# Performance work log

Hardware: AMD Instinct MI355X
Metric: run time of the kernel (lower is better)

The kernel has to match this reference:

```python
import jax, jax.numpy as jnp
import numpy as np

B, T, C = 4, 2048, 1024
QH = 4            # n_q_heads
D = C // QH       # per-head dim = 256
EPS = 1e-5


def setup_inputs() -> dict:
    key = jax.random.key(0)
    k1, k2, k3 = jax.random.split(key, 3)
    residual = jax.random.normal(k1, (B, T, C), dtype=jnp.float32)
    # scale weights ~ Xavier-ish so relu(score)^2 stays numerically sane
    w_fc = jax.random.normal(k2, (C, C), dtype=jnp.float32) * (1.0 / np.sqrt(C))
    w_proj = jax.random.normal(k3, (C, C), dtype=jnp.float32) * (1.0 / np.sqrt(C))
    ln_g = jnp.ones((C,), dtype=jnp.float32)
    ln_b = jnp.zeros((C,), dtype=jnp.float32)
    return {"residual": residual, "w_fc": w_fc, "w_proj": w_proj,
            "ln_g": ln_g, "ln_b": ln_b}


def _layernorm(x, g, b):
    mu = jnp.mean(x, axis=-1, keepdims=True)
    var = jnp.mean(jnp.square(x - mu), axis=-1, keepdims=True)
    return (x - mu) * jax.lax.rsqrt(var + EPS) * g + b


def reference(residual, w_fc, w_proj, ln_g, ln_b):
    Bx, Tx, Cx = residual.shape
    x = _layernorm(residual, ln_g, ln_b)
    # q: (B, QH, T, D)
    q = x.reshape(Bx, Tx, QH, D).transpose(0, 2, 1, 3)
    # keys: rows of w_fc chopped into 4C kv entries of dim D, shared across heads
    k = w_fc.reshape(-1, D)          # (S, D), S = 4C
    # values: columns of w_proj (i.e. w_proj^T rows) chopped the same way
    v = w_proj.T.reshape(-1, D)      # (S, D)
    scores = jnp.einsum('bhtd,sd->bhts', q, k)
    # softmax(log(relusq(score))) then *exp(lse) == plain relu(score)^2 weights
    p = jnp.square(jax.nn.relu(scores))
    out = jnp.einsum('bhts,sd->bhtd', p, v)
    out = out.transpose(0, 2, 1, 3).reshape(Bx, Tx, Cx)
    return residual + out
```

## Files before the change

kernel.cpp:

```cpp
#include <hip/hip_runtime.h>
#include <hip/hip_bf16.h>

typedef __attribute__((ext_vector_type(8))) short bf16x8;
typedef __attribute__((ext_vector_type(4))) float f32x4;

#define C_    1024
#define MROWS 32768
#define D_    256
#define S_TOT 4096
#define SCH   32
#define NCH   (S_TOT / SCH)

__device__ __forceinline__ unsigned short f2bf(float f) {
  union { float f; unsigned int u; } v; v.f = f;
  unsigned int u = v.u;
  u += 0x7fffu + ((u >> 16) & 1u);
  return (unsigned short)(u >> 16);
}

__device__ __forceinline__ void async16(const void* g, void* l) {
  __builtin_amdgcn_global_load_lds(
      (const __attribute__((address_space(1))) unsigned int*)g,
      (__attribute__((address_space(3))) unsigned int*)l, 16, 0, 0);
}

__global__ __launch_bounds__(256) void ln_kernel(const float* __restrict__ res,
                                                 const float* __restrict__ g,
                                                 const float* __restrict__ b,
                                                 unsigned short* __restrict__ xq) {
  int wave = threadIdx.x >> 6, lane = threadIdx.x & 63;
  int row = blockIdx.x * 4 + wave;
  const float* r = res + (size_t)row * C_;
  float4 x[4];
  float s = 0.f, s2 = 0.f;
  #pragma unroll
  for (int i = 0; i < 4; ++i) {
    x[i] = *(const float4*)(r + i * 256 + lane * 4);
    s  += x[i].x + x[i].y + x[i].z + x[i].w;
    s2 += x[i].x * x[i].x + x[i].y * x[i].y + x[i].z * x[i].z + x[i].w * x[i].w;
  }
  #pragma unroll
  for (int off = 32; off > 0; off >>= 1) {
    s  += __shfl_xor(s, off, 64);
    s2 += __shfl_xor(s2, off, 64);
  }
  float mu  = s * (1.0f / C_);
  float var = s2 * (1.0f / C_) - mu * mu;
  float rs  = rsqrtf(var + 1e-5f);
  #pragma unroll
  for (int i = 0; i < 4; ++i) {
    int c = i * 256 + lane * 4;
    float4 gg = *(const float4*)(g + c);
    float4 bb = *(const float4*)(b + c);
    unsigned short o[4];
    o[0] = f2bf((x[i].x - mu) * rs * gg.x + bb.x);
    o[1] = f2bf((x[i].y - mu) * rs * gg.y + bb.y);
    o[2] = f2bf((x[i].z - mu) * rs * gg.z + bb.z);
    o[3] = f2bf((x[i].w - mu) * rs * gg.w + bb.w);
    *(ushort4*)(xq + (size_t)row * C_ + c) = *(ushort4*)o;
  }
}

__global__ __launch_bounds__(256) void prep_k(const float* __restrict__ wfc,
                                              unsigned short* __restrict__ kq) {
  int t = blockIdx.x * 256 + threadIdx.x;
  int lane = t & 63;
  int sn  = (t >> 6) & 1;
  int kc  = (t >> 7) & 7;
  int sc2 = t >> 10;
  int s = sc2 * 32 + sn * 16 + (lane & 15);
  int d = kc * 32 + (lane >> 4) * 8;
  const float* src = wfc + (size_t)s * D_ + d;
  float4 a = *(const float4*)src;
  float4 b = *(const float4*)(src + 4);
  unsigned short o[8] = { f2bf(a.x), f2bf(a.y), f2bf(a.z), f2bf(a.w),
                          f2bf(b.x), f2bf(b.y), f2bf(b.z), f2bf(b.w) };
  *(uint4*)(kq + (size_t)t * 8) = *(uint4*)o;
}

__global__ __launch_bounds__(256) void prep_v(const float* __restrict__ wproj,
                                              unsigned short* __restrict__ vq) {
  __shared__ unsigned short tile[8192];
  int b = blockIdx.x;
  int tid = threadIdx.x;
  int c0 = b * 8;
  #pragma unroll
  for (int it = 0; it < 4; ++it) {
    int row = it * 256 + tid;
    const float* src = wproj + (size_t)row * C_ + c0;
    float4 a = *(const float4*)src;
    float4 bb = *(const float4*)(src + 4);
    unsigned short* dst = &tile[row * 8];
    dst[0] = f2bf(a.x);  dst[1] = f2bf(a.y);  dst[2] = f2bf(a.z);  dst[3] = f2bf(a.w);
    dst[4] = f2bf(bb.x); dst[5] = f2bf(bb.y); dst[6] = f2bf(bb.z); dst[7] = f2bf(bb.w);
  }
  __syncthreads();
  #pragma unroll
  for (int it = 0; it < 4; ++it) {
    int slot = it * 256 + tid;
    int lane = slot & 63;
    int dn   = slot >> 6;
    int d = dn * 16 + (lane & 15);
    int sl0 = (lane >> 4) * 8;
    unsigned short o[8];
    #pragma unroll
    for (int j = 0; j < 8; ++j) {
      int sl = sl0 + j;
      o[j] = tile[((sl & 3) * 256 + d) * 8 + (sl >> 2)];
    }
    *(uint4*)(vq + (size_t)b * 8192 + (size_t)slot * 8) = *(uint4*)o;
  }
}

__global__ __launch_bounds__(512, 2) void mlpmha_main(
    const unsigned short* __restrict__ xq,
    const unsigned short* __restrict__ kq,
    const unsigned short* __restrict__ vq,
    const float* __restrict__ res,
    float* __restrict__ out) {
  __shared__ unsigned short ldsK[2][8192];
  __shared__ unsigned short ldsV[8192];
  __shared__ unsigned short ldsP[128][36];

  int tid  = threadIdx.x;
  int wave = tid >> 6;
  int lane = tid & 63;
  int l16  = lane & 15;
  int quad = lane >> 4;
  int wgM  = blockIdx.x * 128;

  int mi = wave & 3, si = wave >> 2;
  int ni = wave & 3, mi2 = wave >> 2;

  bf16x8 qf[2][8];
  #pragma unroll
  for (int mt = 0; mt < 2; ++mt) {
    const unsigned short* qr =
        xq + (size_t)(wgM + mi * 32 + mt * 16 + l16) * D_ + quad * 8;
    #pragma unroll
    for (int kc = 0; kc < 8; ++kc) qf[mt][kc] = *(const bf16x8*)(qr + kc * 32);
  }

  f32x4 acc[4][4];
  #pragma unroll
  for (int i = 0; i < 4; ++i)
    #pragma unroll
    for (int j = 0; j < 4; ++j) acc[i][j] = (f32x4){0.f, 0.f, 0.f, 0.f};

  int soff = tid * 8;

  {
    const unsigned short* kg = kq + soff;
    async16(kg, &ldsK[0][soff]);
    async16(kg + 4096, &ldsK[0][soff + 4096]);
  }
  __syncthreads();

  for (int sc = 0; sc < NCH; ++sc) {
    int cur = sc & 1;

    {
      const unsigned short* vg = vq + (size_t)sc * 8192 + soff;
      async16(vg, &ldsV[soff]);
      async16(vg + 4096, &ldsV[soff + 4096]);
    }

    f32x4 sacc[2];
    sacc[0] = (f32x4){0.f, 0.f, 0.f, 0.f};
    sacc[1] = (f32x4){0.f, 0.f, 0.f, 0.f};
    #pragma unroll
    for (int kc = 0; kc < 8; ++kc) {
      bf16x8 kb = *(const bf16x8*)&ldsK[cur][(kc * 2 + si) * 512 + lane * 8];
      #pragma unroll
      for (int mt = 0; mt < 2; ++mt)
        sacc[mt] = __builtin_amdgcn_mfma_f32_16x16x32_bf16(qf[mt][kc], kb, sacc[mt], 0, 0, 0);
    }

    #pragma unroll
    for (int mt = 0; mt < 2; ++mt)
      #pragma unroll
      for (int r = 0; r < 4; ++r) {
        float v = sacc[mt][r];
        v = v > 0.f ? v * v : 0.f;
        ldsP[mi * 32 + mt * 16 + quad * 4 + r][si * 16 + l16] = f2bf(v);
      }

    __syncthreads();

    if (sc + 1 < NCH) {
      const unsigned short* kg = kq + (size_t)(sc + 1) * 8192 + soff;
      async16(kg, &ldsK[1 - cur][soff]);
      async16(kg + 4096, &ldsK[1 - cur][soff + 4096]);
    }

    {
      bf16x8 vb[4];
      #pragma unroll
      for (int dnl = 0; dnl < 4; ++dnl)
        vb[dnl] = *(const bf16x8*)&ldsV[((ni * 4 + dnl) * 64 + lane) * 8];
      #pragma unroll
      for (int mt2 = 0; mt2 < 4; ++mt2) {
        const unsigned short* pp = &ldsP[mi2 * 64 + mt2 * 16 + l16][quad * 8];
        union { ushort4 h[2]; bf16x8 v; } pu;
        pu.h[0] = *(const ushort4*)pp;
        pu.h[1] = *(const ushort4*)(pp + 4);
        bf16x8 pa = pu.v;
        #pragma unroll
        for (int dnl = 0; dnl < 4; ++dnl)
          acc[mt2][dnl] = __builtin_amdgcn_mfma_f32_16x16x32_bf16(pa, vb[dnl], acc[mt2][dnl], 0, 0, 0);
      }
    }

    __syncthreads();
  }

  #pragma unroll
  for (int mt2 = 0; mt2 < 4; ++mt2)
    #pragma unroll
    for (int r = 0; r < 4; ++r) {
      size_t row = (size_t)(wgM + mi2 * 64 + mt2 * 16 + quad * 4 + r) * D_;
      #pragma unroll
      for (int dnl = 0; dnl < 4; ++dnl) {
        size_t idx = row + ni * 64 + dnl * 16 + l16;
        out[idx] = res[idx] + acc[mt2][dnl][r];
      }
    }
}

extern "C" void kernel_launch(void* const* d_in, const int* in_sizes, int n_in,
                              void* d_out, int out_size, void* d_ws, size_t ws_size,
                              hipStream_t stream) {
  const float* res   = (const float*)d_in[0];
  const float* wfc   = (const float*)d_in[1];
  const float* wproj = (const float*)d_in[2];
  const float* g     = (const float*)d_in[3];
  const float* b     = (const float*)d_in[4];
  float* out = (float*)d_out;

  unsigned short* xq = (unsigned short*)d_ws;
  unsigned short* kq = xq + (size_t)MROWS * D_;
  unsigned short* vq = kq + (size_t)S_TOT * D_;

  ln_kernel<<<2048, 256, 0, stream>>>(res, g, b, xq);
  prep_k<<<512, 256, 0, stream>>>(wfc, kq);
  prep_v<<<128, 256, 0, stream>>>(wproj, vq);
  mlpmha_main<<<256, 512, 0, stream>>>(xq, kq, vq, res, out);
}
```

Baseline: 242.7 us.

## Double S-chunk to 64 and fuse prep kernels into one launch

The main attention-like kernel now processes 64 kv entries per iteration instead of 32. Each wave covers 64 query rows and a 16-wide S slice, which doubles register-held Q fragments and K/V/P LDS buffers, and halves the number of barrier-separated iterations. The three preprocessing kernels (layernorm, K reformat, V transpose) are merged into one launch that dispatches on block index, removing two launch gaps. The larger LDS footprint and register pressure (qf grows to 32 vectors) may reduce occupancy below the requested two blocks per CU.

Result: slower. 256.7 us (+5.8%).

```diff
diff --git a/kernel.cpp b/kernel.cpp
--- a/kernel.cpp
+++ b/kernel.cpp
@@ -8,7 +8,7 @@
 #define MROWS 32768
 #define D_    256
 #define S_TOT 4096
-#define SCH   32
+#define SCH   64
 #define NCH   (S_TOT / SCH)
 
 __device__ __forceinline__ unsigned short f2bf(float f) {
@@ -24,91 +24,91 @@
       (__attribute__((address_space(3))) unsigned int*)l, 16, 0, 0);
 }
 
-__global__ __launch_bounds__(256) void ln_kernel(const float* __restrict__ res,
-                                                 const float* __restrict__ g,
-                                                 const float* __restrict__ b,
-                                                 unsigned short* __restrict__ xq) {
-  int wave = threadIdx.x >> 6, lane = threadIdx.x & 63;
-  int row = blockIdx.x * 4 + wave;
-  const float* r = res + (size_t)row * C_;
-  float4 x[4];
-  float s = 0.f, s2 = 0.f;
-  #pragma unroll
-  for (int i = 0; i < 4; ++i) {
-    x[i] = *(const float4*)(r + i * 256 + lane * 4);
-    s  += x[i].x + x[i].y + x[i].z + x[i].w;
-    s2 += x[i].x * x[i].x + x[i].y * x[i].y + x[i].z * x[i].z + x[i].w * x[i].w;
-  }
-  #pragma unroll
-  for (int off = 32; off > 0; off >>= 1) {
-    s  += __shfl_xor(s, off, 64);
-    s2 += __shfl_xor(s2, off, 64);
-  }
-  float mu  = s * (1.0f / C_);
-  float var = s2 * (1.0f / C_) - mu * mu;
-  float rs  = rsqrtf(var + 1e-5f);
-  #pragma unroll
-  for (int i = 0; i < 4; ++i) {
-    int c = i * 256 + lane * 4;
-    float4 gg = *(const float4*)(g + c);
-    float4 bb = *(const float4*)(b + c);
-    unsigned short o[4];
-    o[0] = f2bf((x[i].x - mu) * rs * gg.x + bb.x);
-    o[1] = f2bf((x[i].y - mu) * rs * gg.y + bb.y);
-    o[2] = f2bf((x[i].z - mu) * rs * gg.z + bb.z);
-    o[3] = f2bf((x[i].w - mu) * rs * gg.w + bb.w);
-    *(ushort4*)(xq + (size_t)row * C_ + c) = *(ushort4*)o;
-  }
-}
-
-__global__ __launch_bounds__(256) void prep_k(const float* __restrict__ wfc,
-                                              unsigned short* __restrict__ kq) {
-  int t = blockIdx.x * 256 + threadIdx.x;
-  int lane = t & 63;
-  int sn  = (t >> 6) & 1;
-  int kc  = (t >> 7) & 7;
-  int sc2 = t >> 10;
-  int s = sc2 * 32 + sn * 16 + (lane & 15);
-  int d = kc * 32 + (lane >> 4) * 8;
-  const float* src = wfc + (size_t)s * D_ + d;
-  float4 a = *(const float4*)src;
-  float4 b = *(const float4*)(src + 4);
-  unsigned short o[8] = { f2bf(a.x), f2bf(a.y), f2bf(a.z), f2bf(a.w),
-                          f2bf(b.x), f2bf(b.y), f2bf(b.z), f2bf(b.w) };
-  *(uint4*)(kq + (size_t)t * 8) = *(uint4*)o;
-}
-
-__global__ __launch_bounds__(256) void prep_v(const float* __restrict__ wproj,
-                                              unsigned short* __restrict__ vq) {
+__global__ __launch_bounds__(256) void prep_all(
+    const float* __restrict__ res, const float* __restrict__ g,
+    const float* __restrict__ b, const float* __restrict__ wfc,
+    const float* __restrict__ wproj,
+    unsigned short* __restrict__ xq, unsigned short* __restrict__ kq,
+    unsigned short* __restrict__ vq) {
   __shared__ unsigned short tile[8192];
-  int b = blockIdx.x;
+  int bid = blockIdx.x;
   int tid = threadIdx.x;
-  int c0 = b * 8;
-  #pragma unroll
-  for (int it = 0; it < 4; ++it) {
-    int row = it * 256 + tid;
-    const float* src = wproj + (size_t)row * C_ + c0;
+
+  if (bid < 2048) {
+    int wave = tid >> 6, lane = tid & 63;
+    int row = bid * 4 + wave;
+    const float* r = res + (size_t)row * C_;
+    float4 x[4];
+    float s = 0.f, s2 = 0.f;
+    #pragma unroll
+    for (int i = 0; i < 4; ++i) {
+      x[i] = *(const float4*)(r + i * 256 + lane * 4);
+      s  += x[i].x + x[i].y + x[i].z + x[i].w;
+      s2 += x[i].x * x[i].x + x[i].y * x[i].y + x[i].z * x[i].z + x[i].w * x[i].w;
+    }
+    #pragma unroll
+    for (int off = 32; off > 0; off >>= 1) {
+      s  += __shfl_xor(s, off, 64);
+      s2 += __shfl_xor(s2, off, 64);
+    }
+    float mu  = s * (1.0f / C_);
+    float var = s2 * (1.0f / C_) - mu * mu;
+    float rs  = rsqrtf(var + 1e-5f);
+    #pragma unroll
+    for (int i = 0; i < 4; ++i) {
+      int c = i * 256 + lane * 4;
+      float4 gg = *(const float4*)(g + c);
+      float4 bb = *(const float4*)(b + c);
+      unsigned short o[4];
+      o[0] = f2bf((x[i].x - mu) * rs * gg.x + bb.x);
+      o[1] = f2bf((x[i].y - mu) * rs * gg.y + bb.y);
+      o[2] = f2bf((x[i].z - mu) * rs * gg.z + bb.z);
+      o[3] = f2bf((x[i].w - mu) * rs * gg.w + bb.w);
+      *(ushort4*)(xq + (size_t)row * C_ + c) = *(ushort4*)o;
+    }
+  } else if (bid < 2560) {
+    int t = (bid - 2048) * 256 + tid;
+    int lane = t & 63;
+    int sn  = (t >> 6) & 1;
+    int kc  = (t >> 7) & 7;
+    int sc2 = t >> 10;
+    int s = sc2 * 32 + sn * 16 + (lane & 15);
+    int d = kc * 32 + (lane >> 4) * 8;
+    const float* src = wfc + (size_t)s * D_ + d;
     float4 a = *(const float4*)src;
-    float4 bb = *(const float4*)(src + 4);
-    unsigned short* dst = &tile[row * 8];
-    dst[0] = f2bf(a.x);  dst[1] = f2bf(a.y);  dst[2] = f2bf(a.z);  dst[3] = f2bf(a.w);
-    dst[4] = f2bf(bb.x); dst[5] = f2bf(bb.y); dst[6] = f2bf(bb.z); dst[7] = f2bf(bb.w);
-  }
-  __syncthreads();
-  #pragma unroll
-  for (int it = 0; it < 4; ++it) {
-    int slot = it * 256 + tid;
-    int lane = slot & 63;
-    int dn   = slot >> 6;
-    int d = dn * 16 + (lane & 15);
-    int sl0 = (lane >> 4) * 8;
-    unsigned short o[8];
-    #pragma unroll
-    for (int j = 0; j < 8; ++j) {
-      int sl = sl0 + j;
-      o[j] = tile[((sl & 3) * 256 + d) * 8 + (sl >> 2)];
-    }
-    *(uint4*)(vq + (size_t)b * 8192 + (size_t)slot * 8) = *(uint4*)o;
+    float4 b2 = *(const float4*)(src + 4);
+    unsigned short o[8] = { f2bf(a.x), f2bf(a.y), f2bf(a.z), f2bf(a.w),
+                            f2bf(b2.x), f2bf(b2.y), f2bf(b2.z), f2bf(b2.w) };
+    *(uint4*)(kq + (size_t)t * 8) = *(uint4*)o;
+  } else {
+    int bb = bid - 2560;
+    int c0 = bb * 8;
+    #pragma unroll
+    for (int it = 0; it < 4; ++it) {
+      int row = it * 256 + tid;
+      const float* src = wproj + (size_t)row * C_ + c0;
+      float4 a = *(const float4*)src;
+      float4 b2 = *(const float4*)(src + 4);
+      unsigned short* dst = &tile[row * 8];
+      dst[0] = f2bf(a.x);  dst[1] = f2bf(a.y);  dst[2] = f2bf(a.z);  dst[3] = f2bf(a.w);
+      dst[4] = f2bf(b2.x); dst[5] = f2bf(b2.y); dst[6] = f2bf(b2.z); dst[7] = f2bf(b2.w);
+    }
+    __syncthreads();
+    #pragma unroll
+    for (int it = 0; it < 4; ++it) {
+      int slot = it * 256 + tid;
+      int lane = slot & 63;
+      int dn   = slot >> 6;
+      int d = dn * 16 + (lane & 15);
+      int sl0 = (lane >> 4) * 8;
+      unsigned short o[8];
+      #pragma unroll
+      for (int j = 0; j < 8; ++j) {
+        int sl = sl0 + j;
+        o[j] = tile[((sl & 3) * 256 + d) * 8 + (sl >> 2)];
+      }
+      *(uint4*)(vq + (size_t)bb * 8192 + (size_t)slot * 8) = *(uint4*)o;
+    }
   }
 }
 
@@ -118,9 +118,9 @@
     const unsigned short* __restrict__ vq,
     const float* __restrict__ res,
     float* __restrict__ out) {
-  __shared__ unsigned short ldsK[2][8192];
-  __shared__ unsigned short ldsV[8192];
-  __shared__ unsigned short ldsP[128][36];
+  __shared__ unsigned short ldsK[2][16384];
+  __shared__ unsigned short ldsV[16384];
+  __shared__ unsigned short ldsP[2][128][36];
 
   int tid  = threadIdx.x;
   int wave = tid >> 6;
@@ -129,14 +129,15 @@
   int quad = lane >> 4;
   int wgM  = blockIdx.x * 128;
 
-  int mi = wave & 3, si = wave >> 2;
+  int mi = wave & 1, si = wave >> 1;
+  int sh = si >> 1, sl = si & 1;
   int ni = wave & 3, mi2 = wave >> 2;
 
-  bf16x8 qf[2][8];
+  bf16x8 qf[4][8];
   #pragma unroll
-  for (int mt = 0; mt < 2; ++mt) {
+  for (int mt = 0; mt < 4; ++mt) {
     const unsigned short* qr =
-        xq + (size_t)(wgM + mi * 32 + mt * 16 + l16) * D_ + quad * 8;
+        xq + (size_t)(wgM + mi * 64 + mt * 16 + l16) * D_ + quad * 8;
     #pragma unroll
     for (int kc = 0; kc < 8; ++kc) qf[mt][kc] = *(const bf16x8*)(qr + kc * 32);
   }
@@ -151,8 +152,9 @@
 
   {
     const unsigned short* kg = kq + soff;
-    async16(kg, &ldsK[0][soff]);
-    async16(kg + 4096, &ldsK[0][soff + 4096]);
+    #pragma unroll
+    for (int i = 0; i < 4; ++i)
+      async16(kg + i * 4096, &ldsK[0][soff + i * 4096]);
   }
   __syncthreads();
 
@@ -160,50 +162,53 @@
     int cur = sc & 1;
 
     {
-      const unsigned short* vg = vq + (size_t)sc * 8192 + soff;
-      async16(vg, &ldsV[soff]);
-      async16(vg + 4096, &ldsV[soff + 4096]);
-    }
-
-    f32x4 sacc[2];
-    sacc[0] = (f32x4){0.f, 0.f, 0.f, 0.f};
-    sacc[1] = (f32x4){0.f, 0.f, 0.f, 0.f};
+      const unsigned short* vg = vq + (size_t)sc * 16384 + soff;
+      #pragma unroll
+      for (int i = 0; i < 4; ++i)
+        async16(vg + i * 4096, &ldsV[soff + i * 4096]);
+    }
+
+    f32x4 sacc[4];
+    #pragma unroll
+    for (int mt = 0; mt < 4; ++mt) sacc[mt] = (f32x4){0.f, 0.f, 0.f, 0.f};
     #pragma unroll
     for (int kc = 0; kc < 8; ++kc) {
-      bf16x8 kb = *(const bf16x8*)&ldsK[cur][(kc * 2 + si) * 512 + lane * 8];
-      #pragma unroll
-      for (int mt = 0; mt < 2; ++mt)
+      bf16x8 kb = *(const bf16x8*)&ldsK[cur][sh * 8192 + (kc * 2 + sl) * 512 + lane * 8];
+      #pragma unroll
+      for (int mt = 0; mt < 4; ++mt)
         sacc[mt] = __builtin_amdgcn_mfma_f32_16x16x32_bf16(qf[mt][kc], kb, sacc[mt], 0, 0, 0);
     }
 
     #pragma unroll
-    for (int mt = 0; mt < 2; ++mt)
+    for (int mt = 0; mt < 4; ++mt)
       #pragma unroll
       for (int r = 0; r < 4; ++r) {
         float v = sacc[mt][r];
         v = v > 0.f ? v * v : 0.f;
-        ldsP[mi * 32 + mt * 16 + quad * 4 + r][si * 16 + l16] = f2bf(v);
+        ldsP[sh][mi * 64 + mt * 16 + quad * 4 + r][sl * 16 + l16] = f2bf(v);
       }
 
     __syncthreads();
 
     if (sc + 1 < NCH) {
-      const unsigned short* kg = kq + (size_t)(sc + 1) * 8192 + soff;
-      async16(kg, &ldsK[1 - cur][soff]);
-      async16(kg + 4096, &ldsK[1 - cur][soff + 4096]);
-    }
-
-    {
+      const unsigned short* kg = kq + (size_t)(sc + 1) * 16384 + soff;
+      #pragma unroll
+      for (int i = 0; i < 4; ++i)
+        async16(kg + i * 4096, &ldsK[1 - cur][soff + i * 4096]);
+    }
+
+    #pragma unroll
+    for (int h = 0; h < 2; ++h) {
       bf16x8 vb[4];
       #pragma unroll
       for (int dnl = 0; dnl < 4; ++dnl)
-        vb[dnl] = *(const bf16x8*)&ldsV[((ni * 4 + dnl) * 64 + lane) * 8];
+        vb[dnl] = *(const bf16x8*)&ldsV[h * 8192 + ((ni * 4 + dnl) * 64 + lane) * 8];
       #pragma unroll
       for (int mt2 = 0; mt2 < 4; ++mt2) {
-        const unsigned short* pp = &ldsP[mi2 * 64 + mt2 * 16 + l16][quad * 8];
-        union { ushort4 h[2]; bf16x8 v; } pu;
-        pu.h[0] = *(const ushort4*)pp;
-        pu.h[1] = *(const ushort4*)(pp + 4);
+        const unsigned short* pp = &ldsP[h][mi2 * 64 + mt2 * 16 + l16][quad * 8];
+        union { ushort4 u4[2]; bf16x8 v; } pu;
+        pu.u4[0] = *(const ushort4*)pp;
+        pu.u4[1] = *(const ushort4*)(pp + 4);
         bf16x8 pa = pu.v;
         #pragma unroll
         for (int dnl = 0; dnl < 4; ++dnl)
@@ -241,8 +246,6 @@
   unsigned short* kq = xq + (size_t)MROWS * D_;
   unsigned short* vq = kq + (size_t)S_TOT * D_;
 
-  ln_kernel<<<2048, 256, 0, stream>>>(res, g, b, xq);
-  prep_k<<<512, 256, 0, stream>>>(wfc, kq);
-  prep_v<<<128, 256, 0, stream>>>(wproj, vq);
+  prep_all<<<2688, 256, 0, stream>>>(res, g, b, wfc, wproj, xq, kq, vq);
   mlpmha_main<<<256, 512, 0, stream>>>(xq, kq, vq, res, out);
 }
```

## Fuse LayerNorm into main attention kernel and merge K/V prep kernels

Applied to the files above, without the earlier changes.

LayerNorm is now computed inside the main kernel: each workgroup normalizes its 32 tokens into a padded LDS staging area, then loads Q fragments from LDS instead of reading a bf16 activation buffer from global memory. The separate K and V conversion kernels are merged into one launch split by block index. LDS is unified into one buffer that is reused for the Q staging and then the K/V/P tiles. This removes the global round trip for normalized activations and two kernel launches, at the cost of a serial LN prologue in each main-kernel workgroup.

New measurement: 265.9 us. 1.1x slower.

```diff
diff --git a/kernel.cpp b/kernel.cpp
--- a/kernel.cpp
+++ b/kernel.cpp
@@ -24,103 +24,68 @@
       (__attribute__((address_space(3))) unsigned int*)l, 16, 0, 0);
 }
 
-__global__ __launch_bounds__(256) void ln_kernel(const float* __restrict__ res,
-                                                 const float* __restrict__ g,
-                                                 const float* __restrict__ b,
-                                                 unsigned short* __restrict__ xq) {
-  int wave = threadIdx.x >> 6, lane = threadIdx.x & 63;
-  int row = blockIdx.x * 4 + wave;
-  const float* r = res + (size_t)row * C_;
-  float4 x[4];
-  float s = 0.f, s2 = 0.f;
-  #pragma unroll
-  for (int i = 0; i < 4; ++i) {
-    x[i] = *(const float4*)(r + i * 256 + lane * 4);
-    s  += x[i].x + x[i].y + x[i].z + x[i].w;
-    s2 += x[i].x * x[i].x + x[i].y * x[i].y + x[i].z * x[i].z + x[i].w * x[i].w;
-  }
-  #pragma unroll
-  for (int off = 32; off > 0; off >>= 1) {
-    s  += __shfl_xor(s, off, 64);
-    s2 += __shfl_xor(s2, off, 64);
-  }
-  float mu  = s * (1.0f / C_);
-  float var = s2 * (1.0f / C_) - mu * mu;
-  float rs  = rsqrtf(var + 1e-5f);
-  #pragma unroll
-  for (int i = 0; i < 4; ++i) {
-    int c = i * 256 + lane * 4;
-    float4 gg = *(const float4*)(g + c);
-    float4 bb = *(const float4*)(b + c);
-    unsigned short o[4];
-    o[0] = f2bf((x[i].x - mu) * rs * gg.x + bb.x);
-    o[1] = f2bf((x[i].y - mu) * rs * gg.y + bb.y);
-    o[2] = f2bf((x[i].z - mu) * rs * gg.z + bb.z);
-    o[3] = f2bf((x[i].w - mu) * rs * gg.w + bb.w);
-    *(ushort4*)(xq + (size_t)row * C_ + c) = *(ushort4*)o;
-  }
-}
-
-__global__ __launch_bounds__(256) void prep_k(const float* __restrict__ wfc,
-                                              unsigned short* __restrict__ kq) {
-  int t = blockIdx.x * 256 + threadIdx.x;
-  int lane = t & 63;
-  int sn  = (t >> 6) & 1;
-  int kc  = (t >> 7) & 7;
-  int sc2 = t >> 10;
-  int s = sc2 * 32 + sn * 16 + (lane & 15);
-  int d = kc * 32 + (lane >> 4) * 8;
-  const float* src = wfc + (size_t)s * D_ + d;
-  float4 a = *(const float4*)src;
-  float4 b = *(const float4*)(src + 4);
-  unsigned short o[8] = { f2bf(a.x), f2bf(a.y), f2bf(a.z), f2bf(a.w),
-                          f2bf(b.x), f2bf(b.y), f2bf(b.z), f2bf(b.w) };
-  *(uint4*)(kq + (size_t)t * 8) = *(uint4*)o;
-}
-
-__global__ __launch_bounds__(256) void prep_v(const float* __restrict__ wproj,
-                                              unsigned short* __restrict__ vq) {
+__global__ __launch_bounds__(256) void prep_kv(
+    const float* __restrict__ wfc, const float* __restrict__ wproj,
+    unsigned short* __restrict__ kq, unsigned short* __restrict__ vq) {
   __shared__ unsigned short tile[8192];
-  int b = blockIdx.x;
+  int bid = blockIdx.x;
   int tid = threadIdx.x;
-  int c0 = b * 8;
-  #pragma unroll
-  for (int it = 0; it < 4; ++it) {
-    int row = it * 256 + tid;
-    const float* src = wproj + (size_t)row * C_ + c0;
+
+  if (bid < 512) {
+    int t = bid * 256 + tid;
+    int lane = t & 63;
+    int sn  = (t >> 6) & 1;
+    int kc  = (t >> 7) & 7;
+    int sc2 = t >> 10;
+    int s = sc2 * 32 + sn * 16 + (lane & 15);
+    int d = kc * 32 + (lane >> 4) * 8;
+    const float* src = wfc + (size_t)s * D_ + d;
     float4 a = *(const float4*)src;
-    float4 bb = *(const float4*)(src + 4);
-    unsigned short* dst = &tile[row * 8];
-    dst[0] = f2bf(a.x);  dst[1] = f2bf(a.y);  dst[2] = f2bf(a.z);  dst[3] = f2bf(a.w);
-    dst[4] = f2bf(bb.x); dst[5] = f2bf(bb.y); dst[6] = f2bf(bb.z); dst[7] = f2bf(bb.w);
-  }
-  __syncthreads();
-  #pragma unroll
-  for (int it = 0; it < 4; ++it) {
-    int slot = it * 256 + tid;
-    int lane = slot & 63;
-    int dn   = slot >> 6;
-    int d = dn * 16 + (lane & 15);
-    int sl0 = (lane >> 4) * 8;
-    unsigned short o[8];
-    #pragma unroll
-    for (int j = 0; j < 8; ++j) {
-      int sl = sl0 + j;
-      o[j] = tile[((sl & 3) * 256 + d) * 8 + (sl >> 2)];
-    }
-    *(uint4*)(vq + (size_t)b * 8192 + (size_t)slot * 8) = *(uint4*)o;
+    float4 b2 = *(const float4*)(src + 4);
+    unsigned short o[8] = { f2bf(a.x), f2bf(a.y), f2bf(a.z), f2bf(a.w),
+                            f2bf(b2.x), f2bf(b2.y), f2bf(b2.z), f2bf(b2.w) };
+    *(uint4*)(kq + (size_t)t * 8) = *(uint4*)o;
+  } else {
+    int bb = bid - 512;
+    int c0 = bb * 8;
+    #pragma unroll
+    for (int it = 0; it < 4; ++it) {
+      int row = it * 256 + tid;
+      const float* src = wproj + (size_t)row * C_ + c0;
+      float4 a = *(const float4*)src;
+      float4 b2 = *(const float4*)(src + 4);
+      unsigned short* dst = &tile[row * 8];
+      dst[0] = f2bf(a.x);  dst[1] = f2bf(a.y);  dst[2] = f2bf(a.z);  dst[3] = f2bf(a.w);
+      dst[4] = f2bf(b2.x); dst[5] = f2bf(b2.y); dst[6] = f2bf(b2.z); dst[7] = f2bf(b2.w);
+    }
+    __syncthreads();
+    #pragma unroll
+    for (int it = 0; it < 4; ++it) {
+      int slot = it * 256 + tid;
+      int lane = slot & 63;
+      int dn   = slot >> 6;
+      int d = dn * 16 + (lane & 15);
+      int sl0 = (lane >> 4) * 8;
+      unsigned short o[8];
+      #pragma unroll
+      for (int j = 0; j < 8; ++j) {
+        int sl = sl0 + j;
+        o[j] = tile[((sl & 3) * 256 + d) * 8 + (sl >> 2)];
+      }
+      *(uint4*)(vq + (size_t)bb * 8192 + (size_t)slot * 8) = *(uint4*)o;
+    }
   }
 }
 
 __global__ __launch_bounds__(512, 2) void mlpmha_main(
-    const unsigned short* __restrict__ xq,
     const unsigned short* __restrict__ kq,
     const unsigned short* __restrict__ vq,
     const float* __restrict__ res,
+    const float* __restrict__ lng,
+    const float* __restrict__ lnb,
     float* __restrict__ out) {
-  __shared__ unsigned short ldsK[2][8192];
-  __shared__ unsigned short ldsV[8192];
-  __shared__ unsigned short ldsP[128][36];
+  __shared__ __align__(16) unsigned short lds[33792];
+  unsigned short* xl = lds;
 
   int tid  = threadIdx.x;
   int wave = tid >> 6;
@@ -129,17 +94,55 @@
   int quad = lane >> 4;
   int wgM  = blockIdx.x * 128;
 
+  {
+    int tok0 = blockIdx.x * 32;
+    #pragma unroll
+    for (int tt = 0; tt < 4; ++tt) {
+      int tl = wave * 4 + tt;
+      const float* r = res + (size_t)(tok0 + tl) * C_;
+      float4 x[4];
+      float s = 0.f, s2 = 0.f;
+      #pragma unroll
+      for (int i = 0; i < 4; ++i) {
+        x[i] = *(const float4*)(r + i * 256 + lane * 4);
+        s  += x[i].x + x[i].y + x[i].z + x[i].w;
+        s2 += x[i].x * x[i].x + x[i].y * x[i].y + x[i].z * x[i].z + x[i].w * x[i].w;
+      }
+      #pragma unroll
+      for (int off = 32; off > 0; off >>= 1) {
+        s  += __shfl_xor(s, off, 64);
+        s2 += __shfl_xor(s2, off, 64);
+      }
+      float mu  = s * (1.0f / C_);
+      float var = s2 * (1.0f / C_) - mu * mu;
+      float rs  = rsqrtf(var + 1e-5f);
+      #pragma unroll
+      for (int i = 0; i < 4; ++i) {
+        int c = i * 256 + lane * 4;
+        float4 gg = *(const float4*)(lng + c);
+        float4 bb = *(const float4*)(lnb + c);
+        unsigned short o[4];
+        o[0] = f2bf((x[i].x - mu) * rs * gg.x + bb.x);
+        o[1] = f2bf((x[i].y - mu) * rs * gg.y + bb.y);
+        o[2] = f2bf((x[i].z - mu) * rs * gg.z + bb.z);
+        o[3] = f2bf((x[i].w - mu) * rs * gg.w + bb.w);
+        *(ushort4*)(xl + (size_t)(tl * 4 + i) * 264 + lane * 4) = *(ushort4*)o;
+      }
+    }
+  }
+  __syncthreads();
+
   int mi = wave & 3, si = wave >> 2;
   int ni = wave & 3, mi2 = wave >> 2;
 
   bf16x8 qf[2][8];
   #pragma unroll
   for (int mt = 0; mt < 2; ++mt) {
-    const unsigned short* qr =
-        xq + (size_t)(wgM + mi * 32 + mt * 16 + l16) * D_ + quad * 8;
+    const unsigned short* qr = xl + (size_t)(mi * 32 + mt * 16 + l16) * 264 + quad * 8;
     #pragma unroll
     for (int kc = 0; kc < 8; ++kc) qf[mt][kc] = *(const bf16x8*)(qr + kc * 32);
   }
+  __syncthreads();
 
   f32x4 acc[4][4];
   #pragma unroll
@@ -151,8 +154,8 @@
 
   {
     const unsigned short* kg = kq + soff;
-    async16(kg, &ldsK[0][soff]);
-    async16(kg + 4096, &ldsK[0][soff + 4096]);
+    async16(kg, lds + soff);
+    async16(kg + 4096, lds + soff + 4096);
   }
   __syncthreads();
 
@@ -161,8 +164,8 @@
 
     {
       const unsigned short* vg = vq + (size_t)sc * 8192 + soff;
-      async16(vg, &ldsV[soff]);
-      async16(vg + 4096, &ldsV[soff + 4096]);
+      async16(vg, lds + 16384 + soff);
+      async16(vg + 4096, lds + 16384 + soff + 4096);
     }
 
     f32x4 sacc[2];
@@ -170,7 +173,7 @@
     sacc[1] = (f32x4){0.f, 0.f, 0.f, 0.f};
     #pragma unroll
     for (int kc = 0; kc < 8; ++kc) {
-      bf16x8 kb = *(const bf16x8*)&ldsK[cur][(kc * 2 + si) * 512 + lane * 8];
+      bf16x8 kb = *(const bf16x8*)(lds + cur * 8192 + (kc * 2 + si) * 512 + lane * 8);
       #pragma unroll
       for (int mt = 0; mt < 2; ++mt)
         sacc[mt] = __builtin_amdgcn_mfma_f32_16x16x32_bf16(qf[mt][kc], kb, sacc[mt], 0, 0, 0);
@@ -182,28 +185,29 @@
       for (int r = 0; r < 4; ++r) {
         float v = sacc[mt][r];
         v = v > 0.f ? v * v : 0.f;
-        ldsP[mi * 32 + mt * 16 + quad * 4 + r][si * 16 + l16] = f2bf(v);
+        lds[24576 + (mi * 32 + mt * 16 + quad * 4 + r) * 36 + si * 16 + l16] = f2bf(v);
       }
 
     __syncthreads();
 
     if (sc + 1 < NCH) {
       const unsigned short* kg = kq + (size_t)(sc + 1) * 8192 + soff;
-      async16(kg, &ldsK[1 - cur][soff]);
-      async16(kg + 4096, &ldsK[1 - cur][soff + 4096]);
+      async16(kg, lds + (1 - cur) * 8192 + soff);
+      async16(kg + 4096, lds + (1 - cur) * 8192 + soff + 4096);
     }
 
     {
       bf16x8 vb[4];
       #pragma unroll
       for (int dnl = 0; dnl < 4; ++dnl)
-        vb[dnl] = *(const bf16x8*)&ldsV[((ni * 4 + dnl) * 64 + lane) * 8];
+        vb[dnl] = *(const bf16x8*)(lds + 16384 + ((ni * 4 + dnl) * 64 + lane) * 8);
       #pragma unroll
       for (int mt2 = 0; mt2 < 4; ++mt2) {
-        const unsigned short* pp = &ldsP[mi2 * 64 + mt2 * 16 + l16][quad * 8];
-        union { ushort4 h[2]; bf16x8 v; } pu;
-        pu.h[0] = *(const ushort4*)pp;
-        pu.h[1] = *(const ushort4*)(pp + 4);
+        const unsigned short* pp =
+            lds + 24576 + (size_t)(mi2 * 64 + mt2 * 16 + l16) * 36 + quad * 8;
+        union { ushort4 u4[2]; bf16x8 v; } pu;
+        pu.u4[0] = *(const ushort4*)pp;
+        pu.u4[1] = *(const ushort4*)(pp + 4);
         bf16x8 pa = pu.v;
         #pragma unroll
         for (int dnl = 0; dnl < 4; ++dnl)
@@ -237,12 +241,9 @@
   const float* b     = (const float*)d_in[4];
   float* out = (float*)d_out;
 
-  unsigned short* xq = (unsigned short*)d_ws;
-  unsigned short* kq = xq + (size_t)MROWS * D_;
+  unsigned short* kq = (unsigned short*)d_ws;
   unsigned short* vq = kq + (size_t)S_TOT * D_;
 
-  ln_kernel<<<2048, 256, 0, stream>>>(res, g, b, xq);
-  prep_k<<<512, 256, 0, stream>>>(wfc, kq);
-  prep_v<<<128, 256, 0, stream>>>(wproj, vq);
-  mlpmha_main<<<256, 512, 0, stream>>>(xq, kq, vq, res, out);
-}
+  prep_kv<<<640, 256, 0, stream>>>(wfc, wproj, kq, vq);
+  mlpmha_main<<<256, 512, 0, stream>>>(kq, vq, res, g, b, out);
+}
```
